# Kernel optimization log

Hardware: AMD Instinct MI355X
Metric: run time of the kernel (lower is better)

## Reference

```python
import jax, jax.numpy as jnp
import numpy as np

B, T, D = 2, 2048, 2048
H, KV, HD = 16, 4, 128
EPS = 1e-6


def _rmsnorm(x, scale):
    # flax.linen.RMSNorm over last axis: x / sqrt(mean(x^2) + eps) * scale
    var = jnp.mean(jnp.square(x), axis=-1, keepdims=True)
    return x * jax.lax.rsqrt(var + EPS) * scale


def _rope(x, cos, sin):
    # x: [b, t, h, d]; cos/sin: [t, d]
    x_rot = jnp.stack([-x[..., 1::2], x[..., 0::2]], axis=-1)
    x_rot = x_rot.reshape(*x_rot.shape[:-2], -1)
    return x * cos[None, :, None, :] + x_rot * sin[None, :, None, :]


def setup_inputs() -> dict:
    key = jax.random.key(0)
    ks = jax.random.split(key, 5)
    x = jax.random.normal(ks[0], (B, T, D), jnp.float32)
    Wq = jax.random.normal(ks[1], (D, H * HD), jnp.float32) / np.sqrt(D)
    Wk = jax.random.normal(ks[2], (D, KV * HD), jnp.float32) / np.sqrt(D)
    Wv = jax.random.normal(ks[3], (D, KV * HD), jnp.float32) / np.sqrt(D)
    Wo = jax.random.normal(ks[4], (H * HD, D), jnp.float32) / np.sqrt(H * HD)
    q_scale = jnp.ones((HD,), jnp.float32)
    k_scale = jnp.ones((HD,), jnp.float32)
    # standard RoPE tables, interleaved-pair convention
    pos = jnp.arange(T, dtype=jnp.float32)
    inv_freq = 1.0 / (10000.0 ** (jnp.arange(0, HD, 2, dtype=jnp.float32) / HD))
    freqs = pos[:, None] * inv_freq[None, :]  # [T, HD/2]
    cos = jnp.repeat(jnp.cos(freqs), 2, axis=-1)  # [T, HD]
    sin = jnp.repeat(jnp.sin(freqs), 2, axis=-1)
    mask = jnp.tril(jnp.ones((T, T), bool))[None, None]  # causal [1,1,T,T]
    return {"x": x, "Wq": Wq, "Wk": Wk, "Wv": Wv, "Wo": Wo,
            "q_scale": q_scale, "k_scale": k_scale,
            "cos": cos, "sin": sin, "mask": mask}


def reference(x, Wq, Wk, Wv, Wo, q_scale, k_scale, cos, sin, mask):
    num_groups = H // KV
    q = (x @ Wq).reshape(B, T, H, HD)
    k = (x @ Wk).reshape(B, T, KV, HD)
    v = (x @ Wv).reshape(B, T, KV, HD)
    q = _rmsnorm(q, q_scale)
    k = _rmsnorm(k, k_scale)
    q = _rope(q, cos, sin)
    k = _rope(k, cos, sin)
    k = jnp.repeat(k, num_groups, axis=2)  # [b, t, H, d]
    v = jnp.repeat(v, num_groups, axis=2)
    scores = jnp.einsum('bqhd,bkhd->bhqk', q, k) / jnp.sqrt(jnp.float32(HD))
    scores = jnp.where(mask, scores, jnp.finfo(scores.dtype).min)
    attn = jax.nn.softmax(scores, axis=-1)
    out = jnp.einsum('bhqk,bkhd->bqhd', attn, v)
    out = out.reshape(B, T, H * HD)
    return out @ Wo
```

## Files before the change

### kernel.cpp

```cpp
#include <hip/hip_runtime.h>
#include <hip/hip_bf16.h>

#define B_   2
#define T_   2048
#define D_   2048
#define H_   16
#define KV_  4
#define HD_  128
#define BT_  (B_*T_)
#define QKVP 3072
#define KOFF 2048
#define VOFF 2560
static constexpr float EPS_ = 1e-6f;

typedef unsigned short u16;
typedef __attribute__((ext_vector_type(8))) short short8;
typedef __attribute__((ext_vector_type(4))) float f32x4;
typedef __attribute__((ext_vector_type(4))) unsigned short u16x4;

__device__ __forceinline__ u16 f2bf(float f){
    unsigned u = __float_as_uint(f);
    u += 0x7FFF + ((u >> 16) & 1);
    return (u16)(u >> 16);
}
__device__ __forceinline__ float bf2f(u16 u){
    return __uint_as_float((unsigned)u << 16);
}

__device__ __forceinline__ void async_copy16(const void* g, void* l) {
    __builtin_amdgcn_global_load_lds(
        (const __attribute__((address_space(1))) unsigned int*)g,
        (__attribute__((address_space(3))) unsigned int*)l, 16, 0, 0);
}

__global__ __launch_bounds__(256) void cvt_f32_bf16_kernel(
    const float* __restrict__ in, u16* __restrict__ out, int n)
{
    const int i = (blockIdx.x*256 + threadIdx.x)*4;
    if (i < n) {
        float4 v = *(const float4*)&in[i];
        u16x4 w = { f2bf(v.x), f2bf(v.y), f2bf(v.z), f2bf(v.w) };
        *(u16x4*)&out[i] = w;
    }
}

__global__ __launch_bounds__(256) void transpose_cvt_kernel(
    const float* __restrict__ in, u16* __restrict__ out, int R, int C)
{
    __shared__ u16 tile[64][65];
    const int r0 = blockIdx.y*64, c0 = blockIdx.x*64;
    const int tr = threadIdx.x >> 4;
    const int tc = (threadIdx.x & 15) * 4;
    #pragma unroll
    for (int i = 0; i < 4; i++) {
        const int r = tr + i*16;
        float4 v = *(const float4*)&in[(size_t)(r0 + r)*C + c0 + tc];
        tile[tc+0][r] = f2bf(v.x);
        tile[tc+1][r] = f2bf(v.y);
        tile[tc+2][r] = f2bf(v.z);
        tile[tc+3][r] = f2bf(v.w);
    }
    __syncthreads();
    #pragma unroll
    for (int i = 0; i < 4; i++) {
        const int c = tr + i*16;
        u16x4 w = { tile[c][tc+0], tile[c][tc+1], tile[c][tc+2], tile[c][tc+3] };
        *(u16x4*)&out[(size_t)(c0 + c)*R + r0 + tc] = w;
    }
}

__global__ __launch_bounds__(256) void transpose_v_kernel(
    const u16* __restrict__ qkv, u16* __restrict__ vt)
{
    __shared__ u16 tile[64][65];
    const int t0 = blockIdx.x*64;
    const int d0 = blockIdx.y*64;
    const int bk = blockIdx.z;
    const int tr = threadIdx.x >> 4;
    const int tc = (threadIdx.x & 15) * 4;
    #pragma unroll
    for (int i = 0; i < 4; i++) {
        const int t = t0 + tr + i*16;
        u16x4 v = *(const u16x4*)&qkv[(size_t)((bk>>2)*T_ + t)*QKVP + VOFF
                                      + (bk&3)*HD_ + d0 + tc];
        tile[tc+0][tr+i*16] = v[0];
        tile[tc+1][tr+i*16] = v[1];
        tile[tc+2][tr+i*16] = v[2];
        tile[tc+3][tr+i*16] = v[3];
    }
    __syncthreads();
    #pragma unroll
    for (int i = 0; i < 4; i++) {
        const int d = tr + i*16;
        u16x4 w = { tile[d][tc+0], tile[d][tc+1], tile[d][tc+2], tile[d][tc+3] };
        *(u16x4*)&vt[((size_t)bk*HD_ + d0 + d)*T_ + t0 + tc] = w;
    }
}

#define GBM 128
#define GBN 128
#define GBK 32

template<bool OUT_BF16>
__global__ __launch_bounds__(256) void gemm_mfma_kernel(
    const u16* __restrict__ A, const u16* __restrict__ Bt,
    void* __restrict__ C, int N, int K, int lda, int ldb, int ldc)
{
    __shared__ __align__(16) u16 As[GBM][GBK];
    __shared__ __align__(16) u16 Bs[GBN][GBK];
    const int tid  = threadIdx.x;
    const int lane = tid & 63;
    const int wave = tid >> 6;
    const int l15  = lane & 15;
    const int quad = lane >> 4;
    const int wr   = (wave >> 1) * 64;
    const int wc   = (wave & 1) * 64;
    const size_t row0 = (size_t)blockIdx.y * GBM;
    const size_t col0 = (size_t)blockIdx.x * GBN;

    f32x4 acc[4][4];
    #pragma unroll
    for (int i = 0; i < 4; i++)
        #pragma unroll
        for (int j = 0; j < 4; j++)
            acc[i][j] = (f32x4){0.f,0.f,0.f,0.f};

    for (int k0 = 0; k0 < K; k0 += GBK) {
        #pragma unroll
        for (int c = 0; c < 2; c++) {
            const int e = (c*256 + tid) * 8;
            const int r = e >> 5, cc = e & 31;
            async_copy16(A  + (row0 + r)*lda + k0 + cc, &As[r][cc]);
            async_copy16(Bt + (col0 + r)*ldb + k0 + cc, &Bs[r][cc]);
        }
        __syncthreads();

        short8 af[4], bf[4];
        #pragma unroll
        for (int i = 0; i < 4; i++)
            af[i] = *(const short8*)&As[wr + i*16 + l15][quad*8];
        #pragma unroll
        for (int j = 0; j < 4; j++)
            bf[j] = *(const short8*)&Bs[wc + j*16 + l15][quad*8];
        #pragma unroll
        for (int i = 0; i < 4; i++)
            #pragma unroll
            for (int j = 0; j < 4; j++)
                acc[i][j] = __builtin_amdgcn_mfma_f32_16x16x32_bf16(
                    af[i], bf[j], acc[i][j], 0, 0, 0);
        __syncthreads();
    }

    #pragma unroll
    for (int i = 0; i < 4; i++)
        #pragma unroll
        for (int r = 0; r < 4; r++) {
            const size_t row = row0 + wr + i*16 + quad*4 + r;
            #pragma unroll
            for (int j = 0; j < 4; j++) {
                const size_t col = col0 + wc + j*16 + l15;
                if (OUT_BF16) ((u16*)C)[row*ldc + col] = f2bf(acc[i][j][r]);
                else          ((float*)C)[row*ldc + col] = acc[i][j][r];
            }
        }
}

__global__ __launch_bounds__(128) void rmsnorm_rope_kernel(
    u16* __restrict__ qk, const float* __restrict__ scale,
    const float* __restrict__ cosT, const float* __restrict__ sinT,
    int heads_per_token, int head_off, float post_scale)
{
    const int row   = blockIdx.x;
    const int d     = threadIdx.x;
    const int token = row / heads_per_token;
    const int hidx  = row % heads_per_token;
    const int t     = token % T_;
    u16* p = qk + (size_t)token*QKVP + head_off + hidx*HD_;

    float v = bf2f(p[d]);
    __shared__ float red[HD_];
    __shared__ float xs[HD_];
    red[d] = v*v;
    __syncthreads();
    #pragma unroll
    for (int s = 64; s > 0; s >>= 1) {
        if (d < s) red[d] += red[d + s];
        __syncthreads();
    }
    const float rms = rsqrtf(red[0] * (1.0f/HD_) + EPS_);
    const float xn  = v * rms * scale[d];
    xs[d] = xn;
    __syncthreads();
    const float part = xs[d ^ 1];
    const float rot  = (d & 1) ? part : -part;
    p[d] = f2bf((xn*cosT[(size_t)t*HD_ + d] + rot*sinT[(size_t)t*HD_ + d]) * post_scale);
}

#define BQ  64
#define BKV 64

__global__ __launch_bounds__(256, 4) void attn_mfma5_kernel(
    const u16* __restrict__ qkv, const u16* __restrict__ Vtg)
{
    __shared__ __align__(16) u16 Ks[16][BKV][8];
    __shared__ __align__(16) u16 Vt[8][HD_][8];
    __shared__ __align__(16) u16 Pb[4][8][16][8];

    const int pr   = blockIdx.x;
    const int h    = blockIdx.y;
    const int b    = blockIdx.z;
    const int kvh  = h >> 2;
    const int tid  = threadIdx.x;
    const int lane = tid & 63;
    const int wave = tid >> 6;
    const int l15  = lane & 15;
    const int quad = lane >> 4;
    const int NT   = T_ / BQ;

    for (int phase = 0; phase < 2; phase++) {
        const int qt = phase ? pr : (NT - 1 - pr);
        const int q0 = qt * BQ;

        short8 qf[4];
        {
            const u16* qbase = qkv + (size_t)(b*T_ + q0 + wave*16 + l15)*QKVP + h*HD_;
            #pragma unroll
            for (int kt = 0; kt < 4; kt++)
                qf[kt] = *(const short8*)(qbase + (kt*4 + quad)*8);
        }

        float lsum[4] = {0.f, 0.f, 0.f, 0.f};
        f32x4 oacc[8];
        #pragma unroll
        for (int cv = 0; cv < 8; cv++) oacc[cv] = (f32x4){0.f,0.f,0.f,0.f};

        const int ntiles = qt + 1;
        for (int t = 0; t < ntiles; t++) {
            const int k0 = t * BKV;
            __syncthreads();

            #pragma unroll
            for (int it = 0; it < 4; it++) {
                const int n   = it*256 + tid;
                const int cc  = n >> 6;
                const int key = n & 63;
                async_copy16(qkv + (size_t)(b*T_ + k0 + key)*QKVP + KOFF + kvh*HD_ + cc*8,
                             &Ks[cc][key][0]);
            }
            #pragma unroll
            for (int it = 0; it < 4; it++) {
                const int n  = it*256 + tid;
                const int cc = n >> 7;
                const int d  = n & 127;
                async_copy16(Vtg + ((size_t)(b*KV_ + kvh)*HD_ + d)*T_ + k0 + cc*8,
                             &Vt[cc][d][0]);
            }
            __syncthreads();

            f32x4 s[4];
            #pragma unroll
            for (int c = 0; c < 4; c++) s[c] = (f32x4){0.f,0.f,0.f,0.f};
            #pragma unroll
            for (int kt = 0; kt < 4; kt++) {
                #pragma unroll
                for (int c = 0; c < 4; c++) {
                    short8 bf = *(const short8*)&Ks[kt*4 + quad][c*16 + l15][0];
                    s[c] = __builtin_amdgcn_mfma_f32_16x16x32_bf16(qf[kt], bf, s[c], 0, 0, 0);
                }
            }

            if (t == ntiles - 1) {
                const int qrow0 = q0 + wave*16 + quad*4;
                #pragma unroll
                for (int r = 0; r < 4; r++)
                    #pragma unroll
                    for (int c = 0; c < 4; c++) {
                        const int key = k0 + c*16 + l15;
                        if (key > qrow0 + r) s[c][r] = -1e30f;
                    }
            }
            #pragma unroll
            for (int r = 0; r < 4; r++)
                #pragma unroll
                for (int c = 0; c < 4; c++) {
                    const float p = __expf(s[c][r]);
                    s[c][r] = p;
                    lsum[r] += p;
                }

            #pragma unroll
            for (int r = 0; r < 4; r++)
                #pragma unroll
                for (int c = 0; c < 4; c++)
                    Pb[wave][c*2 + (l15 >> 3)][quad*4 + r][l15 & 7] = f2bf(s[c][r]);

            #pragma unroll
            for (int kt2 = 0; kt2 < 2; kt2++) {
                short8 a = *(const short8*)&Pb[wave][kt2*4 + quad][l15][0];
                #pragma unroll
                for (int cv = 0; cv < 8; cv++) {
                    short8 vf = *(const short8*)&Vt[kt2*4 + quad][cv*16 + l15][0];
                    oacc[cv] = __builtin_amdgcn_mfma_f32_16x16x32_bf16(a, vf, oacc[cv], 0, 0, 0);
                }
            }
        }

        #pragma unroll
        for (int r = 0; r < 4; r++) {
            float tot = lsum[r];
            #pragma unroll
            for (int off = 1; off < 16; off <<= 1)
                tot += __shfl_xor(tot, off, 16);
            const float linv = 1.0f / tot;
            u16* orow = (u16*)qkv + (size_t)(b*T_ + q0 + wave*16 + quad*4 + r)*QKVP
                        + h*HD_ + l15;
            #pragma unroll
            for (int cv = 0; cv < 8; cv++)
                orow[cv*16] = f2bf(oacc[cv][r] * linv);
        }
    }
}

extern "C" void kernel_launch(void* const* d_in, const int* in_sizes, int n_in,
                              void* d_out, int out_size, void* d_ws, size_t ws_size,
                              hipStream_t stream)
{
    const float* x    = (const float*)d_in[0];
    const float* Wq   = (const float*)d_in[1];
    const float* Wk   = (const float*)d_in[2];
    const float* Wv   = (const float*)d_in[3];
    const float* Wo   = (const float*)d_in[4];
    const float* qsc  = (const float*)d_in[5];
    const float* ksc  = (const float*)d_in[6];
    const float* cosT = (const float*)d_in[7];
    const float* sinT = (const float*)d_in[8];
    float* out = (float*)d_out;

    u16* xb     = (u16*)d_ws;
    u16* Wqkvt  = xb    + (size_t)BT_*D_;
    u16* Wot    = Wqkvt + (size_t)QKVP*D_;
    u16* qkv    = Wot   + (size_t)D_*(H_*HD_);
    u16* vtg    = qkv   + (size_t)BT_*QKVP;

    cvt_f32_bf16_kernel<<<(BT_*D_)/1024, 256, 0, stream>>>(x, xb, BT_*D_);
    transpose_cvt_kernel<<<dim3((H_*HD_)/64,  D_/64), 256, 0, stream>>>(
        Wq, Wqkvt, D_, H_*HD_);
    transpose_cvt_kernel<<<dim3((KV_*HD_)/64, D_/64), 256, 0, stream>>>(
        Wk, Wqkvt + (size_t)KOFF*D_, D_, KV_*HD_);
    transpose_cvt_kernel<<<dim3((KV_*HD_)/64, D_/64), 256, 0, stream>>>(
        Wv, Wqkvt + (size_t)VOFF*D_, D_, KV_*HD_);
    transpose_cvt_kernel<<<dim3(D_/64, (H_*HD_)/64),  256, 0, stream>>>(
        Wo, Wot, H_*HD_, D_);

    gemm_mfma_kernel<true><<<dim3(QKVP/GBN, BT_/GBM), 256, 0, stream>>>(
        xb, Wqkvt, qkv, QKVP, D_, D_, D_, QKVP);

    rmsnorm_rope_kernel<<<BT_*H_,  HD_, 0, stream>>>(
        qkv, qsc, cosT, sinT, H_, 0, 0.08838834764831845f);
    rmsnorm_rope_kernel<<<BT_*KV_, HD_, 0, stream>>>(
        qkv, ksc, cosT, sinT, KV_, KOFF, 1.0f);

    transpose_v_kernel<<<dim3(T_/64, HD_/64, B_*KV_), 256, 0, stream>>>(qkv, vtg);

    attn_mfma5_kernel<<<dim3(T_/BQ/2, H_, B_), 256, 0, stream>>>(qkv, vtg);

    gemm_mfma_kernel<false><<<dim3(D_/GBN, BT_/GBM), 256, 0, stream>>>(
        qkv, Wot, out, D_, D_, QKVP, D_, D_);
}
```

Before: 395.8 us.

## Double-buffer K/V tiles in attention and use wave-per-head RMSNorm+RoPE

The attention kernel now prefetches the next K/V tile into a second LDS buffer while computing on the current one, and drops one barrier per tile. It also raises wave priority around the MFMA blocks. The doubled LDS lowers the occupancy hint from 4 to 2 blocks per CU. The RMSNorm+RoPE kernel is rewritten to process one head per wavefront with paired elements and shuffle reductions, replacing the shared-memory tree reduction and its many barriers.

```diff
diff --git a/kernel.cpp b/kernel.cpp
--- a/kernel.cpp
+++ b/kernel.cpp
@@ -165,45 +165,44 @@
         }
 }
 
-__global__ __launch_bounds__(128) void rmsnorm_rope_kernel(
+__global__ __launch_bounds__(256) void rmsnorm_rope_kernel(
     u16* __restrict__ qk, const float* __restrict__ scale,
     const float* __restrict__ cosT, const float* __restrict__ sinT,
     int heads_per_token, int head_off, float post_scale)
 {
-    const int row   = blockIdx.x;
-    const int d     = threadIdx.x;
-    const int token = row / heads_per_token;
-    const int hidx  = row % heads_per_token;
-    const int t     = token % T_;
-    u16* p = qk + (size_t)token*QKVP + head_off + hidx*HD_;
-
-    float v = bf2f(p[d]);
-    __shared__ float red[HD_];
-    __shared__ float xs[HD_];
-    red[d] = v*v;
-    __syncthreads();
-    #pragma unroll
-    for (int s = 64; s > 0; s >>= 1) {
-        if (d < s) red[d] += red[d + s];
-        __syncthreads();
-    }
-    const float rms = rsqrtf(red[0] * (1.0f/HD_) + EPS_);
-    const float xn  = v * rms * scale[d];
-    xs[d] = xn;
-    __syncthreads();
-    const float part = xs[d ^ 1];
-    const float rot  = (d & 1) ? part : -part;
-    p[d] = f2bf((xn*cosT[(size_t)t*HD_ + d] + rot*sinT[(size_t)t*HD_ + d]) * post_scale);
+    const int wid   = blockIdx.x*4 + (threadIdx.x >> 6);
+    const int lane  = threadIdx.x & 63;
+    const int token = wid / heads_per_token;
+    const int hidx  = wid % heads_per_token;
+    const int t     = token & (T_ - 1);
+    u16* p = qk + (size_t)token*QKVP + head_off + hidx*HD_ + lane*2;
+
+    const unsigned u = *(const unsigned*)p;
+    const float x0 = bf2f((u16)(u & 0xffff));
+    const float x1 = bf2f((u16)(u >> 16));
+    float ss = x0*x0 + x1*x1;
+    #pragma unroll
+    for (int off = 32; off > 0; off >>= 1) ss += __shfl_xor(ss, off);
+    const float rms = rsqrtf(ss * (1.0f/HD_) + EPS_);
+
+    const float2 sc = *(const float2*)&scale[lane*2];
+    const float2 cs = *(const float2*)&cosT[(size_t)t*HD_ + lane*2];
+    const float2 sn = *(const float2*)&sinT[(size_t)t*HD_ + lane*2];
+    const float n0 = x0 * rms * sc.x;
+    const float n1 = x1 * rms * sc.y;
+    const float r0 = (n0*cs.x - n1*sn.x) * post_scale;
+    const float r1 = (n1*cs.y + n0*sn.y) * post_scale;
+    *(unsigned*)p = (unsigned)f2bf(r0) | ((unsigned)f2bf(r1) << 16);
 }
 
 #define BQ  64
 #define BKV 64
 
-__global__ __launch_bounds__(256, 4) void attn_mfma5_kernel(
+__global__ __launch_bounds__(256, 2) void attn_mfma6_kernel(
     const u16* __restrict__ qkv, const u16* __restrict__ Vtg)
 {
-    __shared__ __align__(16) u16 Ks[16][BKV][8];
-    __shared__ __align__(16) u16 Vt[8][HD_][8];
+    __shared__ __align__(16) u16 Ks[2][16][BKV][8];
+    __shared__ __align__(16) u16 Vt[2][8][HD_][8];
     __shared__ __align__(16) u16 Pb[4][8][16][8];
 
     const int pr   = blockIdx.x;
@@ -235,39 +234,62 @@
         for (int cv = 0; cv < 8; cv++) oacc[cv] = (f32x4){0.f,0.f,0.f,0.f};
 
         const int ntiles = qt + 1;
+
+        #pragma unroll
+        for (int it = 0; it < 4; it++) {
+            const int n   = it*256 + tid;
+            const int cc  = n >> 6;
+            const int key = n & 63;
+            async_copy16(qkv + (size_t)(b*T_ + key)*QKVP + KOFF + kvh*HD_ + cc*8,
+                         &Ks[0][cc][key][0]);
+        }
+        #pragma unroll
+        for (int it = 0; it < 4; it++) {
+            const int n  = it*256 + tid;
+            const int cc = n >> 7;
+            const int d  = n & 127;
+            async_copy16(Vtg + ((size_t)(b*KV_ + kvh)*HD_ + d)*T_ + cc*8,
+                         &Vt[0][cc][d][0]);
+        }
+        __syncthreads();
+
+        int cur = 0;
         for (int t = 0; t < ntiles; t++) {
+            if (t + 1 < ntiles) {
+                const int k0n = (t + 1) * BKV;
+                #pragma unroll
+                for (int it = 0; it < 4; it++) {
+                    const int n   = it*256 + tid;
+                    const int cc  = n >> 6;
+                    const int key = n & 63;
+                    async_copy16(qkv + (size_t)(b*T_ + k0n + key)*QKVP + KOFF + kvh*HD_ + cc*8,
+                                 &Ks[cur^1][cc][key][0]);
+                }
+                #pragma unroll
+                for (int it = 0; it < 4; it++) {
+                    const int n  = it*256 + tid;
+                    const int cc = n >> 7;
+                    const int d  = n & 127;
+                    async_copy16(Vtg + ((size_t)(b*KV_ + kvh)*HD_ + d)*T_ + k0n + cc*8,
+                                 &Vt[cur^1][cc][d][0]);
+                }
+            }
+
             const int k0 = t * BKV;
-            __syncthreads();
-
-            #pragma unroll
-            for (int it = 0; it < 4; it++) {
-                const int n   = it*256 + tid;
-                const int cc  = n >> 6;
-                const int key = n & 63;
-                async_copy16(qkv + (size_t)(b*T_ + k0 + key)*QKVP + KOFF + kvh*HD_ + cc*8,
-                             &Ks[cc][key][0]);
-            }
-            #pragma unroll
-            for (int it = 0; it < 4; it++) {
-                const int n  = it*256 + tid;
-                const int cc = n >> 7;
-                const int d  = n & 127;
-                async_copy16(Vtg + ((size_t)(b*KV_ + kvh)*HD_ + d)*T_ + k0 + cc*8,
-                             &Vt[cc][d][0]);
-            }
-            __syncthreads();
 
             f32x4 s[4];
             #pragma unroll
             for (int c = 0; c < 4; c++) s[c] = (f32x4){0.f,0.f,0.f,0.f};
+            __builtin_amdgcn_s_setprio(1);
             #pragma unroll
             for (int kt = 0; kt < 4; kt++) {
                 #pragma unroll
                 for (int c = 0; c < 4; c++) {
-                    short8 bf = *(const short8*)&Ks[kt*4 + quad][c*16 + l15][0];
+                    short8 bf = *(const short8*)&Ks[cur][kt*4 + quad][c*16 + l15][0];
                     s[c] = __builtin_amdgcn_mfma_f32_16x16x32_bf16(qf[kt], bf, s[c], 0, 0, 0);
                 }
             }
+            __builtin_amdgcn_s_setprio(0);
 
             if (t == ntiles - 1) {
                 const int qrow0 = q0 + wave*16 + quad*4;
@@ -294,15 +316,20 @@
                 for (int c = 0; c < 4; c++)
                     Pb[wave][c*2 + (l15 >> 3)][quad*4 + r][l15 & 7] = f2bf(s[c][r]);
 
+            __builtin_amdgcn_s_setprio(1);
             #pragma unroll
             for (int kt2 = 0; kt2 < 2; kt2++) {
                 short8 a = *(const short8*)&Pb[wave][kt2*4 + quad][l15][0];
                 #pragma unroll
                 for (int cv = 0; cv < 8; cv++) {
-                    short8 vf = *(const short8*)&Vt[kt2*4 + quad][cv*16 + l15][0];
+                    short8 vf = *(const short8*)&Vt[cur][kt2*4 + quad][cv*16 + l15][0];
                     oacc[cv] = __builtin_amdgcn_mfma_f32_16x16x32_bf16(a, vf, oacc[cv], 0, 0, 0);
                 }
             }
+            __builtin_amdgcn_s_setprio(0);
+
+            __syncthreads();
+            cur ^= 1;
         }
 
         #pragma unroll
@@ -355,14 +382,14 @@
     gemm_mfma_kernel<true><<<dim3(QKVP/GBN, BT_/GBM), 256, 0, stream>>>(
         xb, Wqkvt, qkv, QKVP, D_, D_, D_, QKVP);
 
-    rmsnorm_rope_kernel<<<BT_*H_,  HD_, 0, stream>>>(
+    rmsnorm_rope_kernel<<<(BT_*H_)/4,  256, 0, stream>>>(
         qkv, qsc, cosT, sinT, H_, 0, 0.08838834764831845f);
-    rmsnorm_rope_kernel<<<BT_*KV_, HD_, 0, stream>>>(
+    rmsnorm_rope_kernel<<<(BT_*KV_)/4, 256, 0, stream>>>(
         qkv, ksc, cosT, sinT, KV_, KOFF, 1.0f);
 
     transpose_v_kernel<<<dim3(T_/64, HD_/64, B_*KV_), 256, 0, stream>>>(qkv, vtg);
 
-    attn_mfma5_kernel<<<dim3(T_/BQ/2, H_, B_), 256, 0, stream>>>(qkv, vtg);
+    attn_mfma6_kernel<<<dim3(T_/BQ/2, H_, B_), 256, 0, stream>>>(qkv, vtg);
 
     gemm_mfma_kernel<false><<<dim3(D_/GBN, BT_/GBM), 256, 0, stream>>>(
         qkv, Wot, out, D_, D_, QKVP, D_, D_);
```

Measured after the change: 375.3 us. -5.2%, faster.
